# Optimization experiments

Measured on AMD Instinct MI355X. Metric: run time of the kernel, lower is better.

Reference implementation:

```python
import jax, jax.numpy as jnp
import numpy as np
from jax import lax

B, C_IN, H, W = 16, 64, 112, 112
OUP = 128
INIT = 64          # ceil(oup/ratio)
NEW = 64           # init*(ratio-1)
E = 4              # num_experts
SE_HID = (INIT + NEW) // 4
EPS = 1e-5


def setup_inputs() -> dict:
    key = jax.random.key(0)
    ks = jax.random.split(key, 12)
    n = jax.random.normal
    d = {}
    d["x"] = n(ks[0], (B, C_IN, H, W), jnp.float32)
    # DynamicConv 1 (1x1, experts)
    d["rw1"] = n(ks[1], (E, C_IN), jnp.float32) * 0.1
    d["rb1"] = jnp.zeros((E,), jnp.float32)
    d["w1"] = n(ks[2], (E, INIT, C_IN, 1, 1), jnp.float32) / np.sqrt(C_IN)
    d["bn1_g"] = jnp.ones((INIT,), jnp.float32)
    d["bn1_b"] = jnp.zeros((INIT,), jnp.float32)
    d["bn1_m"] = n(ks[3], (INIT,), jnp.float32) * 0.1
    d["bn1_v"] = jax.random.uniform(ks[4], (INIT,), jnp.float32, 0.5, 1.5)
    # DynamicConv 2 (3x3 depthwise, experts)
    d["rw2"] = n(ks[5], (E, INIT), jnp.float32) * 0.1
    d["rb2"] = jnp.zeros((E,), jnp.float32)
    d["w2"] = n(ks[6], (E, NEW, 1, 3, 3), jnp.float32) / 3.0
    d["bn2_g"] = jnp.ones((NEW,), jnp.float32)
    d["bn2_b"] = jnp.zeros((NEW,), jnp.float32)
    d["bn2_m"] = n(ks[7], (NEW,), jnp.float32) * 0.1
    d["bn2_v"] = jax.random.uniform(ks[8], (NEW,), jnp.float32, 0.5, 1.5)
    # AdaptiveSE on INIT+NEW channels
    d["se_w1"] = n(ks[9], (SE_HID, INIT + NEW), jnp.float32) * 0.1
    d["se_b1"] = jnp.zeros((SE_HID,), jnp.float32)
    d["se_w2"] = n(ks[10], (INIT + NEW, SE_HID), jnp.float32) * 0.1
    d["se_b2"] = jnp.zeros((INIT + NEW,), jnp.float32)
    return d


def _bn_relu(x, g, b, m, v):
    # eval-mode BatchNorm2d + ReLU, channel dim = 1
    scale = (g / jnp.sqrt(v + EPS))[None, :, None, None]
    shift = (b - m * g / jnp.sqrt(v + EPS))[None, :, None, None]
    return jax.nn.relu(x * scale + shift)


def reference(x, rw1, rb1, w1, bn1_g, bn1_b, bn1_m, bn1_v,
              rw2, rb2, w2, bn2_g, bn2_b, bn2_m, bn2_v,
              se_w1, se_b1, se_w2, se_b2):
    b = x.shape[0]
    # --- first block: dynamic 1x1 conv ---
    pooled = x.mean((2, 3))                                  # [B, C_IN]
    r1 = jax.nn.sigmoid(pooled @ rw1.T + rb1)                # [B, E]
    # per-sample mixed 1x1 kernel: [B, INIT, C_IN]
    k1 = jnp.einsum('be,eoi->boi', r1, w1[:, :, :, 0, 0])
    x1 = jnp.einsum('boi,bihw->bohw', k1, x)                 # [B, INIT, H, W]
    x1 = _bn_relu(x1, bn1_g, bn1_b, bn1_m, bn1_v)
    # --- second block: dynamic 3x3 depthwise conv ---
    pooled2 = x1.mean((2, 3))                                # [B, INIT]
    r2 = jax.nn.sigmoid(pooled2 @ rw2.T + rb2)               # [B, E]
    k2 = jnp.einsum('be,eokl->bokl', r2, w2[:, :, 0])        # [B, NEW, 3, 3]
    # batched grouped conv: groups = B*INIT (CondConv trick)
    x1r = x1.reshape(1, b * INIT, H, W)
    k2r = k2.reshape(b * NEW, 1, 3, 3)
    x2 = lax.conv_general_dilated(
        x1r, k2r, window_strides=(1, 1), padding=((1, 1), (1, 1)),
        dimension_numbers=('NCHW', 'OIHW', 'NCHW'),
        feature_group_count=b * INIT)
    x2 = x2.reshape(b, NEW, H, W)
    x2 = _bn_relu(x2, bn2_g, bn2_b, bn2_m, bn2_v)
    # --- concat + SE gate ---
    out = jnp.concatenate([x1, x2], axis=1)                  # [B, INIT+NEW, H, W]
    s = out.mean((2, 3))                                     # [B, INIT+NEW]
    s = jax.nn.relu(s @ se_w1.T + se_b1)
    s = jax.nn.sigmoid(s @ se_w2.T + se_b2)
    out = out * s[:, :, None, None]
    return out[:, :OUP]
```

## Files before the change

### kernel.cpp

```cpp
#include <hip/hip_runtime.h>
#include <math.h>

#define NB 16
#define CIN 64
#define HH 112
#define WW 112
#define HW 12544
#define INIT_C 64
#define NEW_C 64
#define NE 4
#define SE_HIDN 32
#define OUTC 128
#define EPSV 1e-5f
#define TP 128
#define NT (HW / TP)

__global__ __launch_bounds__(256) void k_pool(const float* __restrict__ x,
                                              float* __restrict__ pooled,
                                              float* __restrict__ sum1) {
    int bc = blockIdx.x;
    const float4* p4 = (const float4*)(x + (size_t)bc * HW);
    float s = 0.f;
    for (int g = threadIdx.x; g < HW / 4; g += 256) {
        float4 v = p4[g];
        s += v.x + v.y + v.z + v.w;
    }
    for (int off = 32; off > 0; off >>= 1) s += __shfl_down(s, off, 64);
    __shared__ float ls[4];
    if ((threadIdx.x & 63) == 0) ls[threadIdx.x >> 6] = s;
    __syncthreads();
    if (threadIdx.x == 0) {
        pooled[bc] = (ls[0] + ls[1] + ls[2] + ls[3]) * (1.f / (float)HW);
        sum1[bc] = 0.f;
    }
}

__global__ __launch_bounds__(256) void k_conv1(
    const float* __restrict__ x, const float* __restrict__ pooled,
    const float* __restrict__ rw1, const float* __restrict__ rb1,
    const float* __restrict__ w1, const float* __restrict__ bn1_g,
    const float* __restrict__ bn1_b, const float* __restrict__ bn1_m,
    const float* __restrict__ bn1_v, float* __restrict__ out,
    float* __restrict__ sum1) {
    __shared__ alignas(16) float sA[CIN * INIT_C];
    __shared__ alignas(16) float sX[CIN * TP];
    __shared__ float sShift[INIT_C];
    __shared__ float r1s[NE];
    int b = blockIdx.x / NT;
    int tile = blockIdx.x % NT;
    int p0 = tile * TP;
    int t = threadIdx.x;

    if (t < NE) {
        float acc = rb1[t];
        const float* pb = pooled + b * CIN;
        const float* rw = rw1 + t * CIN;
        for (int i = 0; i < CIN; i++) acc = fmaf(pb[i], rw[i], acc);
        r1s[t] = 1.f / (1.f + expf(-acc));
    }
    if (t >= 64 && t < 128) {
        int o = t - 64;
        float sc = bn1_g[o] * rsqrtf(bn1_v[o] + EPSV);
        sShift[o] = bn1_b[o] - bn1_m[o] * sc;
    }
    __syncthreads();

    for (int idx = t; idx < CIN * INIT_C; idx += 256) {
        int o = idx & 63, i = idx >> 6;
        float acc = 0.f;
#pragma unroll
        for (int e = 0; e < NE; e++)
            acc = fmaf(r1s[e], w1[(e * INIT_C + o) * CIN + i], acc);
        float sc = bn1_g[o] * rsqrtf(bn1_v[o] + EPSV);
        sA[i * INIT_C + o] = acc * sc;
    }
    {
        const float* gx = x + (size_t)b * CIN * HW + p0;
        for (int g = t; g < CIN * TP / 4; g += 256) {
            int i = g >> 5, c4 = g & 31;
            ((float4*)sX)[g] = *(const float4*)(gx + (size_t)i * HW + (c4 << 2));
        }
    }
    __syncthreads();

    int pg = t & 31;
    int og = t >> 5;
    float acc[8][4];
#pragma unroll
    for (int u = 0; u < 8; u++)
#pragma unroll
        for (int v = 0; v < 4; v++) acc[u][v] = 0.f;

    const float4* sX4 = (const float4*)sX;
    const float4* sA4 = (const float4*)sA;
#pragma unroll 4
    for (int i = 0; i < CIN; i++) {
        float4 xv = sX4[i * (TP / 4) + pg];
        float4 a0 = sA4[i * (INIT_C / 4) + og * 2];
        float4 a1 = sA4[i * (INIT_C / 4) + og * 2 + 1];
        float av[8] = {a0.x, a0.y, a0.z, a0.w, a1.x, a1.y, a1.z, a1.w};
#pragma unroll
        for (int u = 0; u < 8; u++) {
            acc[u][0] = fmaf(av[u], xv.x, acc[u][0]);
            acc[u][1] = fmaf(av[u], xv.y, acc[u][1]);
            acc[u][2] = fmaf(av[u], xv.z, acc[u][2]);
            acc[u][3] = fmaf(av[u], xv.w, acc[u][3]);
        }
    }

    float csum[8];
#pragma unroll
    for (int u = 0; u < 8; u++) {
        int o = og * 8 + u;
        float sh = sShift[o];
        alignas(16) float r[4];
#pragma unroll
        for (int v = 0; v < 4; v++) r[v] = fmaxf(acc[u][v] + sh, 0.f);
        *(float4*)(out + ((size_t)(b * OUTC + o)) * HW + p0 + pg * 4) =
            *(float4*)r;
        csum[u] = r[0] + r[1] + r[2] + r[3];
    }
#pragma unroll
    for (int u = 0; u < 8; u++) {
        float v = csum[u];
        v += __shfl_xor(v, 16, 64);
        v += __shfl_xor(v, 8, 64);
        v += __shfl_xor(v, 4, 64);
        v += __shfl_xor(v, 2, 64);
        v += __shfl_xor(v, 1, 64);
        if (pg == 0) atomicAdd(&sum1[b * INIT_C + og * 8 + u], v);
    }
}

__global__ __launch_bounds__(256) void k_dwsum(
    const float* __restrict__ xin,
    const float* __restrict__ sum1, const float* __restrict__ rw2,
    const float* __restrict__ rb2, const float* __restrict__ w2,
    const float* __restrict__ bn2_g, const float* __restrict__ bn2_b,
    const float* __restrict__ bn2_m, const float* __restrict__ bn2_v,
    float* __restrict__ sum2) {
    __shared__ alignas(16) float sIn[HW];
    __shared__ float r2s[NE];
    __shared__ float kk[9];
    int c = blockIdx.x & 63;
    int b = blockIdx.x >> 6;
    int t = threadIdx.x;

    if (t < NE) {
        float acc = rb2[t];
        const float* s1 = sum1 + b * INIT_C;
        const float* rw = rw2 + t * INIT_C;
        for (int i = 0; i < INIT_C; i++)
            acc = fmaf(s1[i] * (1.f / (float)HW), rw[i], acc);
        r2s[t] = 1.f / (1.f + expf(-acc));
    }
    __syncthreads();
    if (t < 9) {
        float acc = 0.f;
#pragma unroll
        for (int e = 0; e < NE; e++)
            acc = fmaf(r2s[e], w2[(e * NEW_C + c) * 9 + t], acc);
        kk[t] = acc * (bn2_g[c] * rsqrtf(bn2_v[c] + EPSV));
    }
    const float4* src4 = (const float4*)(xin + ((size_t)(b * OUTC + c)) * HW);
    for (int g = t; g < HW / 4; g += 256) ((float4*)sIn)[g] = src4[g];
    __syncthreads();

    float sc2 = bn2_g[c] * rsqrtf(bn2_v[c] + EPSV);
    float shift = bn2_b[c] - bn2_m[c] * sc2;
    float myk[9];
#pragma unroll
    for (int j = 0; j < 9; j++) myk[j] = kk[j];

    float csum = 0.f;
    for (int g = t; g < HW / 4; g += 256) {
        int rr = g / (WW / 4);
        int c4 = (g % (WW / 4)) << 2;
#pragma unroll
        for (int v = 0; v < 4; v++) {
            int col = c4 + v;
            float acc = 0.f;
#pragma unroll
            for (int dy = 0; dy < 3; dy++) {
                int ir = rr + dy - 1;
                bool rok = (ir >= 0) && (ir < HH);
#pragma unroll
                for (int dx = 0; dx < 3; dx++) {
                    int cc = col + dx - 1;
                    float xv = (rok && cc >= 0 && cc < WW) ? sIn[ir * WW + cc] : 0.f;
                    acc = fmaf(xv, myk[dy * 3 + dx], acc);
                }
            }
            csum += fmaxf(acc + shift, 0.f);
        }
    }
    for (int off = 32; off > 0; off >>= 1) csum += __shfl_down(csum, off, 64);
    __shared__ float ls[4];
    if ((t & 63) == 0) ls[t >> 6] = csum;
    __syncthreads();
    if (t == 0) sum2[b * NEW_C + c] = ls[0] + ls[1] + ls[2] + ls[3];
}

__global__ __launch_bounds__(256) void k_final(
    const float* __restrict__ xin, const float* __restrict__ sum1,
    const float* __restrict__ sum2, const float* __restrict__ rw2,
    const float* __restrict__ rb2, const float* __restrict__ w2,
    const float* __restrict__ bn2_g, const float* __restrict__ bn2_b,
    const float* __restrict__ bn2_m, const float* __restrict__ bn2_v,
    const float* __restrict__ se_w1, const float* __restrict__ se_b1,
    const float* __restrict__ se_w2, const float* __restrict__ se_b2,
    float* __restrict__ out) {
    __shared__ alignas(16) float sIn[HW];
    __shared__ float sin_[OUTC];
    __shared__ float hvec[SE_HIDN];
    __shared__ float r2s[NE];
    __shared__ float kk[9];
    int c = blockIdx.x & 63;
    int b = blockIdx.x >> 6;
    int t = threadIdx.x;

    if (t < 64) sin_[t] = sum1[b * 64 + t] * (1.f / (float)HW);
    else if (t < 128) sin_[t] = sum2[b * 64 + (t - 64)] * (1.f / (float)HW);
    if (t >= 128 && t < 128 + NE) {
        int e = t - 128;
        float acc = rb2[e];
        const float* s1 = sum1 + b * INIT_C;
        const float* rw = rw2 + e * INIT_C;
        for (int i = 0; i < INIT_C; i++)
            acc = fmaf(s1[i] * (1.f / (float)HW), rw[i], acc);
        r2s[e] = 1.f / (1.f + expf(-acc));
    }
    __syncthreads();
    if (t < SE_HIDN) {
        float acc = se_b1[t];
        const float* wrow = se_w1 + t * OUTC;
#pragma unroll 4
        for (int i = 0; i < OUTC; i++) acc = fmaf(sin_[i], wrow[i], acc);
        hvec[t] = fmaxf(acc, 0.f);
    }
    if (t >= 64 && t < 73) {
        int j = t - 64;
        float acc = 0.f;
#pragma unroll
        for (int e = 0; e < NE; e++)
            acc = fmaf(r2s[e], w2[(e * NEW_C + c) * 9 + j], acc);
        kk[j] = acc * (bn2_g[c] * rsqrtf(bn2_v[c] + EPSV));
    }
    const float4* src4 = (const float4*)(xin + ((size_t)(b * OUTC + c)) * HW);
    for (int g = t; g < HW / 4; g += 256) ((float4*)sIn)[g] = src4[g];
    __syncthreads();
    float a1 = se_b2[c], a2 = se_b2[64 + c];
    {
        const float* w2a = se_w2 + c * SE_HIDN;
        const float* w2b = se_w2 + (64 + c) * SE_HIDN;
#pragma unroll 8
        for (int j = 0; j < SE_HIDN; j++) {
            float hj = hvec[j];
            a1 = fmaf(hj, w2a[j], a1);
            a2 = fmaf(hj, w2b[j], a2);
        }
    }
    float s1v = 1.f / (1.f + expf(-a1));
    float s2v = 1.f / (1.f + expf(-a2));
    float sc2 = bn2_g[c] * rsqrtf(bn2_v[c] + EPSV);
    float shift = bn2_b[c] - bn2_m[c] * sc2;
    float myk[9];
#pragma unroll
    for (int j = 0; j < 9; j++) myk[j] = kk[j];

    float* d1 = out + ((size_t)(b * OUTC + c)) * HW;
    float* d2 = out + ((size_t)(b * OUTC + 64 + c)) * HW;
    for (int g = t; g < HW / 4; g += 256) {
        int rr = g / (WW / 4);
        int c4 = (g % (WW / 4)) << 2;
        alignas(16) float o1[4], o2[4];
#pragma unroll
        for (int v = 0; v < 4; v++) {
            int col = c4 + v;
            float acc = 0.f;
#pragma unroll
            for (int dy = 0; dy < 3; dy++) {
                int ir = rr + dy - 1;
                bool rok = (ir >= 0) && (ir < HH);
#pragma unroll
                for (int dx = 0; dx < 3; dx++) {
                    int cc = col + dx - 1;
                    float xv = (rok && cc >= 0 && cc < WW) ? sIn[ir * WW + cc] : 0.f;
                    acc = fmaf(xv, myk[dy * 3 + dx], acc);
                }
            }
            float x2v = fmaxf(acc + shift, 0.f);
            o1[v] = sIn[rr * WW + col] * s1v;
            o2[v] = x2v * s2v;
        }
        *(float4*)(d1 + (size_t)rr * WW + c4) = *(float4*)o1;
        *(float4*)(d2 + (size_t)rr * WW + c4) = *(float4*)o2;
    }
}

extern "C" void kernel_launch(void* const* d_in, const int* in_sizes, int n_in,
                              void* d_out, int out_size, void* d_ws,
                              size_t ws_size, hipStream_t stream) {
    (void)in_sizes; (void)n_in; (void)out_size; (void)ws_size;
    const float* x = (const float*)d_in[0];
    const float* rw1 = (const float*)d_in[1];
    const float* rb1 = (const float*)d_in[2];
    const float* w1 = (const float*)d_in[3];
    const float* bn1_g = (const float*)d_in[4];
    const float* bn1_b = (const float*)d_in[5];
    const float* bn1_m = (const float*)d_in[6];
    const float* bn1_v = (const float*)d_in[7];
    const float* rw2 = (const float*)d_in[8];
    const float* rb2 = (const float*)d_in[9];
    const float* w2 = (const float*)d_in[10];
    const float* bn2_g = (const float*)d_in[11];
    const float* bn2_b = (const float*)d_in[12];
    const float* bn2_m = (const float*)d_in[13];
    const float* bn2_v = (const float*)d_in[14];
    const float* se_w1 = (const float*)d_in[15];
    const float* se_b1 = (const float*)d_in[16];
    const float* se_w2 = (const float*)d_in[17];
    const float* se_b2 = (const float*)d_in[18];
    float* out = (float*)d_out;
    float* ws = (float*)d_ws;
    float* pooled = ws;
    float* sum1 = ws + 1024;
    float* sum2 = ws + 2048;

    k_pool<<<NB * CIN, 256, 0, stream>>>(x, pooled, sum1);
    k_conv1<<<NB * NT, 256, 0, stream>>>(x, pooled, rw1, rb1, w1, bn1_g, bn1_b,
                                         bn1_m, bn1_v, out, sum1);
    k_dwsum<<<NB * NEW_C, 256, 0, stream>>>(out, sum1, rw2, rb2, w2, bn2_g,
                                            bn2_b, bn2_m, bn2_v, sum2);
    k_final<<<NB * NEW_C, 256, 0, stream>>>(out, sum1, sum2, rw2, rb2, w2,
                                            bn2_g, bn2_b, bn2_m, bn2_v, se_w1,
                                            se_b1, se_w2, se_b2, out);
}
```

Measured before the change: 334.7 us.

## Hoist mixed-kernel prep, enlarge conv1 tiles, use sliding-row depthwise conv

Adds a separate k_prep kernel that builds the per-sample mixed 1x1 weights once per batch, instead of every conv1 block recomputing them from w1. conv1 now processes 256 pixels per block with an 8x8 register tile, cutting blocks and shared-memory traffic per FMA. The depthwise 3x3 in both dwsum and final is rewritten to use a zero-padded shared buffer and a rolling three-row register window per thread, which removes per-tap bounds checks and reloads. The costs are an extra launch, larger register pressure (launch_bounds 256,2), and 4 of every 32 threads idle in the depthwise kernels.

```diff
diff --git a/kernel.cpp b/kernel.cpp
--- a/kernel.cpp
+++ b/kernel.cpp
@@ -12,8 +12,8 @@
 #define SE_HIDN 32
 #define OUTC 128
 #define EPSV 1e-5f
-#define TP 128
-#define NT (HW / TP)
+#define TPX 256
+#define NT (HW / TPX)
 
 __global__ __launch_bounds__(256) void k_pool(const float* __restrict__ x,
                                               float* __restrict__ pooled,
@@ -35,22 +35,14 @@
     }
 }
 
-__global__ __launch_bounds__(256) void k_conv1(
-    const float* __restrict__ x, const float* __restrict__ pooled,
-    const float* __restrict__ rw1, const float* __restrict__ rb1,
-    const float* __restrict__ w1, const float* __restrict__ bn1_g,
-    const float* __restrict__ bn1_b, const float* __restrict__ bn1_m,
-    const float* __restrict__ bn1_v, float* __restrict__ out,
-    float* __restrict__ sum1) {
-    __shared__ alignas(16) float sA[CIN * INIT_C];
-    __shared__ alignas(16) float sX[CIN * TP];
-    __shared__ float sShift[INIT_C];
+__global__ __launch_bounds__(256) void k_prep(
+    const float* __restrict__ pooled, const float* __restrict__ rw1,
+    const float* __restrict__ rb1, const float* __restrict__ w1,
+    const float* __restrict__ bn1_g, const float* __restrict__ bn1_v,
+    float* __restrict__ k1t) {
+    int b = blockIdx.x;
+    int t = threadIdx.x;
     __shared__ float r1s[NE];
-    int b = blockIdx.x / NT;
-    int tile = blockIdx.x % NT;
-    int p0 = tile * TP;
-    int t = threadIdx.x;
-
     if (t < NE) {
         float acc = rb1[t];
         const float* pb = pooled + b * CIN;
@@ -58,13 +50,7 @@
         for (int i = 0; i < CIN; i++) acc = fmaf(pb[i], rw[i], acc);
         r1s[t] = 1.f / (1.f + expf(-acc));
     }
-    if (t >= 64 && t < 128) {
-        int o = t - 64;
-        float sc = bn1_g[o] * rsqrtf(bn1_v[o] + EPSV);
-        sShift[o] = bn1_b[o] - bn1_m[o] * sc;
-    }
-    __syncthreads();
-
+    __syncthreads();
     for (int idx = t; idx < CIN * INIT_C; idx += 256) {
         int o = idx & 63, i = idx >> 6;
         float acc = 0.f;
@@ -72,40 +58,63 @@
         for (int e = 0; e < NE; e++)
             acc = fmaf(r1s[e], w1[(e * INIT_C + o) * CIN + i], acc);
         float sc = bn1_g[o] * rsqrtf(bn1_v[o] + EPSV);
-        sA[i * INIT_C + o] = acc * sc;
+        k1t[b * (CIN * INIT_C) + idx] = acc * sc;
+    }
+}
+
+__global__ __launch_bounds__(256, 2) void k_conv1(
+    const float* __restrict__ x, const float* __restrict__ k1t,
+    const float* __restrict__ bn1_g, const float* __restrict__ bn1_b,
+    const float* __restrict__ bn1_m, const float* __restrict__ bn1_v,
+    float* __restrict__ out, float* __restrict__ sum1) {
+    __shared__ alignas(16) float sA[CIN * INIT_C];
+    __shared__ alignas(16) float sX[CIN * TPX];
+    __shared__ float sShift[INIT_C];
+    int b = blockIdx.x / NT;
+    int tile = blockIdx.x % NT;
+    int p0 = tile * TPX;
+    int t = threadIdx.x;
+
+    {
+        const float4* src = (const float4*)(k1t + (size_t)b * CIN * INIT_C);
+        for (int g = t; g < CIN * INIT_C / 4; g += 256) ((float4*)sA)[g] = src[g];
+    }
+    if (t < INIT_C) {
+        float sc = bn1_g[t] * rsqrtf(bn1_v[t] + EPSV);
+        sShift[t] = bn1_b[t] - bn1_m[t] * sc;
     }
     {
         const float* gx = x + (size_t)b * CIN * HW + p0;
-        for (int g = t; g < CIN * TP / 4; g += 256) {
-            int i = g >> 5, c4 = g & 31;
+        for (int g = t; g < CIN * TPX / 4; g += 256) {
+            int i = g >> 6, c4 = g & 63;
             ((float4*)sX)[g] = *(const float4*)(gx + (size_t)i * HW + (c4 << 2));
         }
     }
     __syncthreads();
 
+    int og = t >> 5;
     int pg = t & 31;
-    int og = t >> 5;
-    float acc[8][4];
+    float acc[8][8];
 #pragma unroll
     for (int u = 0; u < 8; u++)
 #pragma unroll
-        for (int v = 0; v < 4; v++) acc[u][v] = 0.f;
-
+        for (int v = 0; v < 8; v++) acc[u][v] = 0.f;
+
+    const float4* sA4 = (const float4*)sA;
     const float4* sX4 = (const float4*)sX;
-    const float4* sA4 = (const float4*)sA;
-#pragma unroll 4
+#pragma unroll 2
     for (int i = 0; i < CIN; i++) {
-        float4 xv = sX4[i * (TP / 4) + pg];
         float4 a0 = sA4[i * (INIT_C / 4) + og * 2];
         float4 a1 = sA4[i * (INIT_C / 4) + og * 2 + 1];
+        float4 x0 = sX4[i * (TPX / 4) + pg];
+        float4 x1 = sX4[i * (TPX / 4) + 32 + pg];
         float av[8] = {a0.x, a0.y, a0.z, a0.w, a1.x, a1.y, a1.z, a1.w};
-#pragma unroll
-        for (int u = 0; u < 8; u++) {
-            acc[u][0] = fmaf(av[u], xv.x, acc[u][0]);
-            acc[u][1] = fmaf(av[u], xv.y, acc[u][1]);
-            acc[u][2] = fmaf(av[u], xv.z, acc[u][2]);
-            acc[u][3] = fmaf(av[u], xv.w, acc[u][3]);
-        }
+        float xv[8] = {x0.x, x0.y, x0.z, x0.w, x1.x, x1.y, x1.z, x1.w};
+#pragma unroll
+        for (int u = 0; u < 8; u++)
+#pragma unroll
+            for (int v = 0; v < 8; v++)
+                acc[u][v] = fmaf(av[u], xv[v], acc[u][v]);
     }
 
     float csum[8];
@@ -113,12 +122,16 @@
     for (int u = 0; u < 8; u++) {
         int o = og * 8 + u;
         float sh = sShift[o];
-        alignas(16) float r[4];
-#pragma unroll
-        for (int v = 0; v < 4; v++) r[v] = fmaxf(acc[u][v] + sh, 0.f);
-        *(float4*)(out + ((size_t)(b * OUTC + o)) * HW + p0 + pg * 4) =
-            *(float4*)r;
-        csum[u] = r[0] + r[1] + r[2] + r[3];
+        alignas(16) float r0[4], r1[4];
+#pragma unroll
+        for (int v = 0; v < 4; v++) {
+            r0[v] = fmaxf(acc[u][v] + sh, 0.f);
+            r1[v] = fmaxf(acc[u][4 + v] + sh, 0.f);
+        }
+        float* dst = out + ((size_t)(b * OUTC + o)) * HW + p0;
+        *(float4*)(dst + pg * 4) = *(float4*)r0;
+        *(float4*)(dst + 128 + pg * 4) = *(float4*)r1;
+        csum[u] = r0[0] + r0[1] + r0[2] + r0[3] + r1[0] + r1[1] + r1[2] + r1[3];
     }
 #pragma unroll
     for (int u = 0; u < 8; u++) {
@@ -132,16 +145,51 @@
     }
 }
 
+__device__ __forceinline__ void ldrow(const float* __restrict__ sP, int pr,
+                                      int cg, float4& C, float& L, float& R) {
+    const float* row = sP + pr * WW;
+    C = *(const float4*)(row + cg * 4);
+    int lc = cg * 4 - 1;
+    lc = lc < 0 ? 0 : lc;
+    float lv = row[lc];
+    L = (cg == 0) ? 0.f : lv;
+    int rc = cg * 4 + 4;
+    rc = rc > (WW - 1) ? (WW - 1) : rc;
+    float rv = row[rc];
+    R = (cg == 27) ? 0.f : rv;
+}
+
+__device__ __forceinline__ float4 dw9(const float4 c0, float l0, float r0,
+                                      const float4 c1, float l1, float r1,
+                                      const float4 c2, float l2, float r2,
+                                      const float* __restrict__ K) {
+    float4 o;
+    o.x = fmaf(K[0], l0, fmaf(K[1], c0.x, fmaf(K[2], c0.y,
+          fmaf(K[3], l1, fmaf(K[4], c1.x, fmaf(K[5], c1.y,
+          fmaf(K[6], l2, fmaf(K[7], c2.x, K[8] * c2.y))))))));
+    o.y = fmaf(K[0], c0.x, fmaf(K[1], c0.y, fmaf(K[2], c0.z,
+          fmaf(K[3], c1.x, fmaf(K[4], c1.y, fmaf(K[5], c1.z,
+          fmaf(K[6], c2.x, fmaf(K[7], c2.y, K[8] * c2.z))))))));
+    o.z = fmaf(K[0], c0.y, fmaf(K[1], c0.z, fmaf(K[2], c0.w,
+          fmaf(K[3], c1.y, fmaf(K[4], c1.z, fmaf(K[5], c1.w,
+          fmaf(K[6], c2.y, fmaf(K[7], c2.z, K[8] * c2.w))))))));
+    o.w = fmaf(K[0], c0.z, fmaf(K[1], c0.w, fmaf(K[2], r0,
+          fmaf(K[3], c1.z, fmaf(K[4], c1.w, fmaf(K[5], r1,
+          fmaf(K[6], c2.z, fmaf(K[7], c2.w, K[8] * r2))))))));
+    return o;
+}
+
+#define PROWS (HH + 2)
+
 __global__ __launch_bounds__(256) void k_dwsum(
-    const float* __restrict__ xin,
-    const float* __restrict__ sum1, const float* __restrict__ rw2,
-    const float* __restrict__ rb2, const float* __restrict__ w2,
-    const float* __restrict__ bn2_g, const float* __restrict__ bn2_b,
-    const float* __restrict__ bn2_m, const float* __restrict__ bn2_v,
-    float* __restrict__ sum2) {
-    __shared__ alignas(16) float sIn[HW];
+    const float* __restrict__ xin, const float* __restrict__ sum1,
+    const float* __restrict__ rw2, const float* __restrict__ rb2,
+    const float* __restrict__ w2, const float* __restrict__ bn2_g,
+    const float* __restrict__ bn2_b, const float* __restrict__ bn2_m,
+    const float* __restrict__ bn2_v, float* __restrict__ sum2) {
+    __shared__ alignas(16) float sP[PROWS * WW];
     __shared__ float r2s[NE];
-    __shared__ float kk[9];
+    __shared__ float kks[9];
     int c = blockIdx.x & 63;
     int b = blockIdx.x >> 6;
     int t = threadIdx.x;
@@ -154,44 +202,47 @@
             acc = fmaf(s1[i] * (1.f / (float)HW), rw[i], acc);
         r2s[t] = 1.f / (1.f + expf(-acc));
     }
+    if (t < WW / 4) {
+        float4 z = {0.f, 0.f, 0.f, 0.f};
+        ((float4*)sP)[t] = z;
+        ((float4*)(sP + (PROWS - 1) * WW))[t] = z;
+    }
     __syncthreads();
     if (t < 9) {
         float acc = 0.f;
 #pragma unroll
         for (int e = 0; e < NE; e++)
             acc = fmaf(r2s[e], w2[(e * NEW_C + c) * 9 + t], acc);
-        kk[t] = acc * (bn2_g[c] * rsqrtf(bn2_v[c] + EPSV));
+        kks[t] = acc * (bn2_g[c] * rsqrtf(bn2_v[c] + EPSV));
     }
     const float4* src4 = (const float4*)(xin + ((size_t)(b * OUTC + c)) * HW);
-    for (int g = t; g < HW / 4; g += 256) ((float4*)sIn)[g] = src4[g];
+    float4* dst4 = (float4*)(sP + WW);
+    for (int g = t; g < HW / 4; g += 256) dst4[g] = src4[g];
     __syncthreads();
 
     float sc2 = bn2_g[c] * rsqrtf(bn2_v[c] + EPSV);
     float shift = bn2_b[c] - bn2_m[c] * sc2;
     float myk[9];
 #pragma unroll
-    for (int j = 0; j < 9; j++) myk[j] = kk[j];
-
+    for (int j = 0; j < 9; j++) myk[j] = kks[j];
+
+    int cg = t & 31;
+    int band = t >> 5;
     float csum = 0.f;
-    for (int g = t; g < HW / 4; g += 256) {
-        int rr = g / (WW / 4);
-        int c4 = (g % (WW / 4)) << 2;
-#pragma unroll
-        for (int v = 0; v < 4; v++) {
-            int col = c4 + v;
-            float acc = 0.f;
-#pragma unroll
-            for (int dy = 0; dy < 3; dy++) {
-                int ir = rr + dy - 1;
-                bool rok = (ir >= 0) && (ir < HH);
-#pragma unroll
-                for (int dx = 0; dx < 3; dx++) {
-                    int cc = col + dx - 1;
-                    float xv = (rok && cc >= 0 && cc < WW) ? sIn[ir * WW + cc] : 0.f;
-                    acc = fmaf(xv, myk[dy * 3 + dx], acc);
-                }
-            }
-            csum += fmaxf(acc + shift, 0.f);
+    if (cg < 28) {
+        int pr0 = band * 14;
+        float4 C[3];
+        float L[3], R[3];
+        ldrow(sP, pr0, cg, C[0], L[0], R[0]);
+        ldrow(sP, pr0 + 1, cg, C[1], L[1], R[1]);
+#pragma unroll
+        for (int k = 0; k < 14; k++) {
+            int s0 = k % 3, s1 = (k + 1) % 3, s2 = (k + 2) % 3;
+            ldrow(sP, pr0 + k + 2, cg, C[s2], L[s2], R[s2]);
+            float4 o = dw9(C[s0], L[s0], R[s0], C[s1], L[s1], R[s1],
+                           C[s2], L[s2], R[s2], myk);
+            csum += fmaxf(o.x + shift, 0.f) + fmaxf(o.y + shift, 0.f) +
+                    fmaxf(o.z + shift, 0.f) + fmaxf(o.w + shift, 0.f);
         }
     }
     for (int off = 32; off > 0; off >>= 1) csum += __shfl_down(csum, off, 64);
@@ -210,11 +261,11 @@
     const float* __restrict__ se_w1, const float* __restrict__ se_b1,
     const float* __restrict__ se_w2, const float* __restrict__ se_b2,
     float* __restrict__ out) {
-    __shared__ alignas(16) float sIn[HW];
+    __shared__ alignas(16) float sP[PROWS * WW];
     __shared__ float sin_[OUTC];
     __shared__ float hvec[SE_HIDN];
     __shared__ float r2s[NE];
-    __shared__ float kk[9];
+    __shared__ float kks[9];
     int c = blockIdx.x & 63;
     int b = blockIdx.x >> 6;
     int t = threadIdx.x;
@@ -230,6 +281,11 @@
             acc = fmaf(s1[i] * (1.f / (float)HW), rw[i], acc);
         r2s[e] = 1.f / (1.f + expf(-acc));
     }
+    if (t >= 160 && t < 160 + WW / 4) {
+        float4 z = {0.f, 0.f, 0.f, 0.f};
+        ((float4*)sP)[t - 160] = z;
+        ((float4*)(sP + (PROWS - 1) * WW))[t - 160] = z;
+    }
     __syncthreads();
     if (t < SE_HIDN) {
         float acc = se_b1[t];
@@ -244,10 +300,11 @@
 #pragma unroll
         for (int e = 0; e < NE; e++)
             acc = fmaf(r2s[e], w2[(e * NEW_C + c) * 9 + j], acc);
-        kk[j] = acc * (bn2_g[c] * rsqrtf(bn2_v[c] + EPSV));
+        kks[j] = acc * (bn2_g[c] * rsqrtf(bn2_v[c] + EPSV));
     }
     const float4* src4 = (const float4*)(xin + ((size_t)(b * OUTC + c)) * HW);
-    for (int g = t; g < HW / 4; g += 256) ((float4*)sIn)[g] = src4[g];
+    float4* pdst4 = (float4*)(sP + WW);
+    for (int g = t; g < HW / 4; g += 256) pdst4[g] = src4[g];
     __syncthreads();
     float a1 = se_b2[c], a2 = se_b2[64 + c];
     {
@@ -266,35 +323,36 @@
     float shift = bn2_b[c] - bn2_m[c] * sc2;
     float myk[9];
 #pragma unroll
-    for (int j = 0; j < 9; j++) myk[j] = kk[j];
-
-    float* d1 = out + ((size_t)(b * OUTC + c)) * HW;
-    float* d2 = out + ((size_t)(b * OUTC + 64 + c)) * HW;
-    for (int g = t; g < HW / 4; g += 256) {
-        int rr = g / (WW / 4);
-        int c4 = (g % (WW / 4)) << 2;
-        alignas(16) float o1[4], o2[4];
-#pragma unroll
-        for (int v = 0; v < 4; v++) {
-            int col = c4 + v;
-            float acc = 0.f;
-#pragma unroll
-            for (int dy = 0; dy < 3; dy++) {
-                int ir = rr + dy - 1;
-                bool rok = (ir >= 0) && (ir < HH);
-#pragma unroll
-                for (int dx = 0; dx < 3; dx++) {
-                    int cc = col + dx - 1;
-                    float xv = (rok && cc >= 0 && cc < WW) ? sIn[ir * WW + cc] : 0.f;
-                    acc = fmaf(xv, myk[dy * 3 + dx], acc);
-                }
-            }
-            float x2v = fmaxf(acc + shift, 0.f);
-            o1[v] = sIn[rr * WW + col] * s1v;
-            o2[v] = x2v * s2v;
-        }
-        *(float4*)(d1 + (size_t)rr * WW + c4) = *(float4*)o1;
-        *(float4*)(d2 + (size_t)rr * WW + c4) = *(float4*)o2;
+    for (int j = 0; j < 9; j++) myk[j] = kks[j];
+
+    int cg = t & 31;
+    int band = t >> 5;
+    if (cg < 28) {
+        float* d1 = out + ((size_t)(b * OUTC + c)) * HW;
+        float* d2 = out + ((size_t)(b * OUTC + 64 + c)) * HW;
+        int pr0 = band * 14;
+        float4 C[3];
+        float L[3], R[3];
+        ldrow(sP, pr0, cg, C[0], L[0], R[0]);
+        ldrow(sP, pr0 + 1, cg, C[1], L[1], R[1]);
+#pragma unroll
+        for (int k = 0; k < 14; k++) {
+            int s0 = k % 3, s1 = (k + 1) % 3, s2 = (k + 2) % 3;
+            ldrow(sP, pr0 + k + 2, cg, C[s2], L[s2], R[s2]);
+            float4 o = dw9(C[s0], L[s0], R[s0], C[s1], L[s1], R[s1],
+                           C[s2], L[s2], R[s2], myk);
+            float4 x1v = C[s1];
+            float4 o1, o2;
+            o1.x = x1v.x * s1v; o1.y = x1v.y * s1v;
+            o1.z = x1v.z * s1v; o1.w = x1v.w * s1v;
+            o2.x = fmaxf(o.x + shift, 0.f) * s2v;
+            o2.y = fmaxf(o.y + shift, 0.f) * s2v;
+            o2.z = fmaxf(o.z + shift, 0.f) * s2v;
+            o2.w = fmaxf(o.w + shift, 0.f) * s2v;
+            int row = band * 14 + k;
+            *(float4*)(d1 + (size_t)row * WW + cg * 4) = o1;
+            *(float4*)(d2 + (size_t)row * WW + cg * 4) = o2;
+        }
     }
 }
 
@@ -326,10 +384,12 @@
     float* pooled = ws;
     float* sum1 = ws + 1024;
     float* sum2 = ws + 2048;
+    float* k1t = ws + 3072;
 
     k_pool<<<NB * CIN, 256, 0, stream>>>(x, pooled, sum1);
-    k_conv1<<<NB * NT, 256, 0, stream>>>(x, pooled, rw1, rb1, w1, bn1_g, bn1_b,
-                                         bn1_m, bn1_v, out, sum1);
+    k_prep<<<NB, 256, 0, stream>>>(pooled, rw1, rb1, w1, bn1_g, bn1_v, k1t);
+    k_conv1<<<NB * NT, 256, 0, stream>>>(x, k1t, bn1_g, bn1_b, bn1_m, bn1_v,
+                                         out, sum1);
     k_dwsum<<<NB * NEW_C, 256, 0, stream>>>(out, sum1, rw2, rb2, w2, bn2_g,
                                             bn2_b, bn2_m, bn2_v, sum2);
     k_final<<<NB * NEW_C, 256, 0, stream>>>(out, sum1, sum2, rw2, rb2, w2,
```

After: 307.6 us. 1.09x faster.
